# Optimization experiments

Hardware: AMD Instinct MI355X
Metric: run time of the kernel (lower is better)

The kernel has to match this reference:

```python
import jax, jax.numpy as jnp
import numpy as np
import math

DIM = 1536
N_HEADS = 12
HEAD_DIM = DIM // N_HEADS  # 128
C = HEAD_DIM // 2          # 64 complex rotation channels
CT = C - 2 * (C // 3)      # 22 temporal channels
CH = C // 3                # 21 height channels
CW = C // 3                # 21 width channels
F, H, W = 3, 30, 52        # video latent grid -> S = 4680
S = F * H * W
B = 1
EPS = 1e-6
NEG = -1e30


def _rope_angles(max_pos, sizes):
    # Wan-style rope_params per axis: theta_j = 10000^(-j/m) for m complex dims
    parts = []
    pos = jnp.arange(max_pos, dtype=jnp.float32)
    for m in sizes:
        inv = 10000.0 ** (-jnp.arange(m, dtype=jnp.float32) / m)
        parts.append(pos[:, None] * inv[None, :])
    return jnp.concatenate(parts, axis=-1)  # [max_pos, C]


def setup_inputs() -> dict:
    key = jax.random.key(0)
    ks = jax.random.split(key, 6)
    sc = 0.02
    inp = {
        'x': jax.random.normal(ks[0], (B, S, DIM), jnp.float32),
        'seq_lens': jnp.array([S], dtype=jnp.int32),
        'grid_sizes': jnp.array([[F, H, W]], dtype=jnp.int32),
        'freqs': _rope_angles(1024, [CT, CH, CW]),  # [1024, 64] rotation angles
        'Wq': jax.random.normal(ks[1], (DIM, DIM), jnp.float32) * sc,
        'bq': jnp.zeros((DIM,), jnp.float32),
        'Wk': jax.random.normal(ks[2], (DIM, DIM), jnp.float32) * sc,
        'bk': jnp.zeros((DIM,), jnp.float32),
        'Wv': jax.random.normal(ks[3], (DIM, DIM), jnp.float32) * sc,
        'bv': jnp.zeros((DIM,), jnp.float32),
        'Wo': jax.random.normal(ks[4], (DIM, DIM), jnp.float32) * sc,
        'bo': jnp.zeros((DIM,), jnp.float32),
        'gq': jnp.ones((DIM,), jnp.float32),
        'gk': jnp.ones((DIM,), jnp.float32),
    }
    return inp


def _rmsnorm(x, g):
    return x * jax.lax.rsqrt(jnp.mean(x * x, axis=-1, keepdims=True) + EPS) * g


def _apply_rope(x, grid_sizes, freqs):
    # x: [B, S, n, d]; rotate consecutive pairs by 3D (t,h,w) factorized angles.
    b, s, n, d = x.shape
    f = grid_sizes[0, 0]
    h = grid_sizes[0, 1]
    w = grid_sizes[0, 2]
    pos = jnp.arange(s)
    t_idx = pos // (h * w)
    y_idx = (pos % (h * w)) // w
    x_idx = pos % w
    ang = jnp.concatenate([
        freqs[t_idx, :CT],
        freqs[y_idx, CT:CT + CH],
        freqs[x_idx, CT + CH:],
    ], axis=-1)  # [S, C]
    cos = jnp.cos(ang)[None, :, None, :]  # [1, S, 1, C]
    sin = jnp.sin(ang)[None, :, None, :]
    xp = x.reshape(b, s, n, d // 2, 2)
    xr, xi = xp[..., 0], xp[..., 1]
    out_r = xr * cos - xi * sin
    out_i = xr * sin + xi * cos
    return jnp.stack([out_r, out_i], axis=-1).reshape(b, s, n, d)


def reference(x, seq_lens, grid_sizes, freqs, Wq, bq, Wk, bk, Wv, bv, Wo, bo, gq, gk):
    b, s, _ = x.shape
    n, d = N_HEADS, HEAD_DIM
    q = _rmsnorm(x @ Wq.T + bq, gq).reshape(b, s, n, d)
    k = _rmsnorm(x @ Wk.T + bk, gk).reshape(b, s, n, d)
    v = (x @ Wv.T + bv).reshape(b, s, n, d)

    rq = _apply_rope(q, grid_sizes, freqs)
    rk = _apply_rope(k, grid_sizes, freqs)

    # frame-level block-causal mask (block_mask in the original flex_attention)
    frame_seqlen = grid_sizes[0, 1] * grid_sizes[0, 2]
    frame_id = jnp.arange(s) // frame_seqlen
    allowed = frame_id[:, None] >= frame_id[None, :]  # [S, S]

    scale = 1.0 / math.sqrt(d)
    scores = jnp.einsum('bqnd,bknd->bnqk', rq, rk) * scale
    scores = jnp.where(allowed[None, None], scores, NEG)
    attn = jax.nn.softmax(scores, axis=-1)
    out = jnp.einsum('bnqk,bknd->bqnd', attn, v).reshape(b, s, n * d)
    return out @ Wo.T + bo
```

## Files before the change

kernel.cpp:

```cpp
#include <hip/hip_runtime.h>
#include <hip/hip_bf16.h>
#include <math.h>
#include <stdint.h>

#define S_LEN 4680
#define DIMSZ 1536
#define NH    12
#define HD    128
#define FRAME 1560
#define NGRP  74
#define PANH  (NGRP * 8192)
#define NSLOT 150

typedef _Float16 f16;
typedef _Float16 f16x8 __attribute__((ext_vector_type(8)));
typedef _Float16 f16x4 __attribute__((ext_vector_type(4)));
typedef _Float16 f16x2 __attribute__((ext_vector_type(2)));
typedef __fp16   fp16x2 __attribute__((ext_vector_type(2)));
typedef float    f32x4  __attribute__((ext_vector_type(4)));
typedef float    f32x16 __attribute__((ext_vector_type(16)));
typedef int      v2i    __attribute__((ext_vector_type(2)));

__device__ __forceinline__ void async16(const void* g, void* l) {
    __builtin_amdgcn_global_load_lds((const __attribute__((address_space(1))) void*)g,
                                     (__attribute__((address_space(3))) void*)l, 16, 0, 0);
}

__device__ __forceinline__ float fexp2(float x) {
#if __has_builtin(__builtin_amdgcn_exp2f)
    return __builtin_amdgcn_exp2f(x);
#else
    return exp2f(x);
#endif
}

union PkCast { fp16x2 v; int i; };
union FragCast { int w[4]; f16x8 v; };

__global__ __launch_bounds__(256) void cast_all(const float* __restrict__ x,
                                                const float* __restrict__ wq,
                                                const float* __restrict__ wk,
                                                const float* __restrict__ wv,
                                                const float* __restrict__ wo,
                                                f16* __restrict__ xh,
                                                f16* __restrict__ wh) {
    int y = blockIdx.y;
    int i = blockIdx.x * 256 + threadIdx.x;
    if (y == 0) {
        if (i < (S_LEN * DIMSZ) / 4) {
            float4 v = ((const float4*)x)[i];
            f16x4 h; h[0]=(f16)v.x; h[1]=(f16)v.y; h[2]=(f16)v.z; h[3]=(f16)v.w;
            ((f16x4*)xh)[i] = h;
        }
    } else {
        const int nW4 = (DIMSZ * DIMSZ) / 4;
        if (i < nW4) {
            const float* src = (y==1)?wq:(y==2)?wk:(y==3)?wv:wo;
            float4 v = ((const float4*)src)[i];
            f16x4 h; h[0]=(f16)v.x; h[1]=(f16)v.y; h[2]=(f16)v.z; h[3]=(f16)v.w;
            ((f16x4*)wh)[(size_t)(y-1)*nW4 + i] = h;
        }
    }
}

__global__ __launch_bounds__(256) void gemm_qkv(const f16* __restrict__ A,
                                                const f16* __restrict__ Bq,
                                                const f16* __restrict__ Bk,
                                                const f16* __restrict__ Bv,
                                                const float* __restrict__ bq,
                                                const float* __restrict__ bk,
                                                const float* __restrict__ bv,
                                                f16* __restrict__ preq,
                                                f16* __restrict__ prek,
                                                f16* __restrict__ vtp) {
    int z = blockIdx.z;
    const f16* B = (z==0) ? Bq : (z==1) ? Bk : Bv;
    const float* bias = (z==0) ? bq : (z==1) ? bk : bv;

    __shared__ __align__(16) f16 Al[128 * 64];
    __shared__ __align__(16) f16 Bl[128 * 64];
    int tid = threadIdx.x;
    int lane = tid & 63, wv = tid >> 6;
    int l16 = lane & 15, quad = lane >> 4;
    int wr = (wv >> 1) * 64, wc = (wv & 1) * 64;
    int m0 = blockIdx.x * 128, n0 = blockIdx.y * 128;

    f32x4 acc[4][4] = {};

    for (int kb = 0; kb < DIMSZ; kb += 64) {
        __syncthreads();
#pragma unroll
        for (int j = 0; j < 4; j++) {
            int s = j * 256 + wv * 64 + lane;
            int r = s >> 3, cc = s & 7;
            const f16* src = A + (size_t)min(m0 + r, S_LEN - 1) * DIMSZ + kb + ((cc ^ (r & 7)) << 3);
            async16(src, (char*)Al + (j * 4096 + wv * 1024));
        }
#pragma unroll
        for (int j = 0; j < 4; j++) {
            int s = j * 256 + wv * 64 + lane;
            int r = s >> 3, cc = s & 7;
            const f16* src = B + (size_t)(n0 + r) * DIMSZ + kb + ((cc ^ (r & 7)) << 3);
            async16(src, (char*)Bl + (j * 4096 + wv * 1024));
        }
        __builtin_amdgcn_s_waitcnt(0x0f70);
        __syncthreads();

#pragma unroll
        for (int kc = 0; kc < 2; kc++) {
            f16x8 af[4], bf[4];
#pragma unroll
            for (int i = 0; i < 4; i++) {
                int ar = wr + i * 16 + l16;
                af[i] = *(const f16x8*)((const char*)Al + ar * 128 + (((kc * 4 + quad) ^ (ar & 7)) << 4));
                int br = wc + i * 16 + l16;
                bf[i] = *(const f16x8*)((const char*)Bl + br * 128 + (((kc * 4 + quad) ^ (br & 7)) << 4));
            }
#pragma unroll
            for (int mi = 0; mi < 4; mi++)
#pragma unroll
                for (int ni = 0; ni < 4; ni++)
                    acc[mi][ni] = __builtin_amdgcn_mfma_f32_16x16x32_f16(af[mi], bf[ni], acc[mi][ni], 0, 0, 0);
        }
    }

    if (z < 2) {
        f16* C = (z == 0) ? preq : prek;
#pragma unroll
        for (int mi = 0; mi < 4; mi++)
#pragma unroll
            for (int ni = 0; ni < 4; ni++) {
                int col = n0 + wc + ni * 16 + l16;
                float bv_ = bias[col];
#pragma unroll
                for (int r = 0; r < 4; r++) {
                    int row = m0 + wr + mi * 16 + quad * 4 + r;
                    if (row < S_LEN) C[(size_t)row * DIMSZ + col] = (f16)(acc[mi][ni][r] + bv_);
                }
            }
    } else {
#pragma unroll
        for (int mi = 0; mi < 4; mi++)
#pragma unroll
            for (int ni = 0; ni < 4; ni++) {
                int col  = n0 + wc + ni * 16 + l16;
                int vhead = col >> 7, d = col & 127;
                int base = m0 + wr + mi * 16 + quad * 4;
                if (base < S_LEN) {
                    float bv_ = bias[col];
                    f16x4 h;
#pragma unroll
                    for (int r = 0; r < 4; r++) h[r] = (f16)(acc[mi][ni][r] + bv_);
                    size_t off = (size_t)vhead * PANH + (size_t)(base >> 6) * 8192
                               + ((base >> 3) & 7) * 1024 + d * 8 + (base & 7);
                    *(f16x4*)(vtp + off) = h;
                }
            }
    }
}

__global__ __launch_bounds__(256) void norm_rope(const f16* __restrict__ preq,
                                                 const f16* __restrict__ prek,
                                                 const float* __restrict__ gq,
                                                 const float* __restrict__ gk,
                                                 const float* __restrict__ freqs,
                                                 f16* __restrict__ Qp,
                                                 f16* __restrict__ Kp) {
    int s = blockIdx.x, which = blockIdx.y;
    int t = threadIdx.x;
    const f16* pre = which ? prek : preq;
    const float* g = which ? gk : gq;
    f16* dst = which ? Kp : Qp;
    const f16* row = pre + (size_t)s * DIMSZ + t * 6;

    float v[6];
    float ss = 0.f;
#pragma unroll
    for (int i = 0; i < 3; i++) {
        f16x2 hp = *(const f16x2*)(row + 2 * i);
        v[2*i] = (float)hp[0]; v[2*i+1] = (float)hp[1];
        ss += v[2*i]*v[2*i] + v[2*i+1]*v[2*i+1];
    }
#pragma unroll
    for (int off = 32; off; off >>= 1) ss += __shfl_xor(ss, off);
    __shared__ float red[4];
    if ((t & 63) == 0) red[t >> 6] = ss;
    __syncthreads();
    float tot = red[0] + red[1] + red[2] + red[3];
    float rms = rsqrtf(tot * (1.0f / DIMSZ) + 1e-6f);

    int tpos = s / FRAME;
    int rem  = s % FRAME;
    int ypos = rem / 52;
    int xpos = s % 52;

#pragma unroll
    for (int u = 0; u < 3; u++) {
        int c = t * 6 + u * 2;
        int head = c >> 7;
        int d = c & 127;
        int j = d >> 1;
        int idx = (j < 22) ? tpos : ((j < 43) ? ypos : xpos);
        float ang = freqs[idx * 64 + j];
        float sn, cs;
        __sincosf(ang, &sn, &cs);
        float vr = v[u * 2]     * rms * g[c];
        float vi = v[u * 2 + 1] * rms * g[c + 1];
        f16* o = dst + (size_t)head * PANH + (size_t)(s >> 6) * 8192
               + (d >> 3) * 512 + (s & 63) * 8 + (d & 7);
        o[0] = (f16)(vr * cs - vi * sn);
        o[1] = (f16)(vr * sn + vi * cs);
    }
}

__global__ __launch_bounds__(128, 2) void attn_part(const f16* __restrict__ Qp,
                                                    const f16* __restrict__ Kp,
                                                    const f16* __restrict__ Vp,
                                                    f16* __restrict__ Opart,
                                                    float* __restrict__ lpart) {
    int bx = blockIdx.x, head = blockIdx.y;
    int t, c, NC2;
    if (bx < 24)      { t = bx >> 1;             c = bx & 1;       NC2 = 2; }
    else if (bx < 72) { t = 12 + ((bx - 24) >> 2); c = (bx - 24) & 3; NC2 = 4; }
    else              { t = 24 + (bx - 72) / 6;  c = (bx - 72) % 6; NC2 = 6; }

    int qlast = min(t * 128 + 127, S_LEN - 1);
    int nfrm  = qlast / FRAME + 1;
    int kvend = nfrm * FRAME; if (kvend > S_LEN) kvend = S_LEN;
    int nG    = (kvend + 63) >> 6;
    int g0 = (c * nG) / NC2, g1 = ((c + 1) * nG) / NC2;
    int limB = ((t * 128) / FRAME + 1) * FRAME;

    int tid = threadIdx.x, lane = tid & 63, wv = tid >> 6;
    int l31 = lane & 31, lh = lane >> 5;
    int qw = t * 128 + wv * 64;

    __shared__ __align__(16) char smem[32768];
    const char* smc = smem;

    const f16* Qg = Qp + ((size_t)head * NGRP + (qw >> 6)) * 8192;
    f16x8 bqf[2][8];
#pragma unroll
    for (int nt = 0; nt < 2; nt++)
#pragma unroll
        for (int ks = 0; ks < 8; ks++) {
            f16x8 vq = *(const f16x8*)(Qg + (2 * ks + lh) * 512 + (l31 + 32 * nt) * 8);
            bqf[nt][ks] = vq * (f16)0.12752044581f;
        }

    int lim[2];
#pragma unroll
    for (int nt = 0; nt < 2; nt++) {
        int q = qw + l31 + 32 * nt;
        lim[nt] = (q / FRAME + 1) * FRAME;
    }

    f32x16 oacc[4][2] = {};
    float lp[2] = {0.f, 0.f};

    int koff = lh * 1024 + l31 * 16;
    int voff = lh * 2048 + l31 * 16;

    const f16* Kh = Kp + (size_t)head * NGRP * 8192;
    const f16* Vh = Vp + (size_t)head * NGRP * 8192;

    for (int g = g0; g < g1; g++) {
        int kb = g * 64;
#pragma unroll
        for (int i = 0; i < 8; i++) {
            int s = i * 2 + wv;
            async16(Kh + (size_t)g * 8192 + s * 512 + lane * 8,
                    (char*)smem + s * 1024 + lane * 16);
        }
#pragma unroll
        for (int i = 0; i < 8; i++) {
            int s = i * 2 + wv;
            async16(Vh + (size_t)g * 8192 + s * 512 + lane * 8,
                    (char*)smem + 16384 + s * 1024 + lane * 16);
        }
        __builtin_amdgcn_s_waitcnt(0x0f70);
        __builtin_amdgcn_s_barrier();

        bool domask = (kb + 64 > limB);

#pragma unroll
        for (int kt = 0; kt < 2; kt++) {
            f32x16 sc0 = {}, sc1 = {};
            __builtin_amdgcn_s_setprio(1);
#pragma unroll
            for (int h = 0; h < 2; h++) {
                f16x8 ka[4];
#pragma unroll
                for (int i = 0; i < 4; i++)
                    ka[i] = *(const f16x8*)(smc + koff + (h * 4 + i) * 2048 + kt * 512);
#pragma unroll
                for (int i = 0; i < 4; i++) {
                    sc0 = __builtin_amdgcn_mfma_f32_32x32x16_f16(ka[i], bqf[0][h*4+i], sc0, 0, 0, 0);
                    sc1 = __builtin_amdgcn_mfma_f32_32x32x16_f16(ka[i], bqf[1][h*4+i], sc1, 0, 0, 0);
                }
            }
            __builtin_amdgcn_s_setprio(0);

            int w[2][8];
            int keyb = kb + kt * 32 + 4 * lh;
#pragma unroll
            for (int nt = 0; nt < 2; nt++) {
#pragma unroll
                for (int p = 0; p < 8; p++) {
                    const int r0 = 2 * p;
                    float s0 = (nt == 0) ? sc0[r0]     : sc1[r0];
                    float s1 = (nt == 0) ? sc0[r0 + 1] : sc1[r0 + 1];
                    if (domask) {
                        int k0 = keyb + (r0 & 3) + 8 * (r0 >> 2);
                        if (k0     >= lim[nt]) s0 = -1e30f;
                        if (k0 + 1 >= lim[nt]) s1 = -1e30f;
                    }
                    float p0 = fexp2(s0), p1 = fexp2(s1);
                    lp[nt] += p0 + p1;
                    PkCast pk; pk.v = __builtin_amdgcn_cvt_pkrtz(p0, p1);
                    w[nt][p] = pk.i;
                }
            }

            f16x8 pb[2][2];
#pragma unroll
            for (int nt = 0; nt < 2; nt++)
#pragma unroll
                for (int ks = 0; ks < 2; ks++) {
                    FragCast fc;
#if __has_builtin(__builtin_amdgcn_permlane32_swap)
                    v2i r02 = __builtin_amdgcn_permlane32_swap(w[nt][4*ks+0], w[nt][4*ks+2], false, false);
                    v2i r13 = __builtin_amdgcn_permlane32_swap(w[nt][4*ks+1], w[nt][4*ks+3], false, false);
                    fc.w[0] = r02.x; fc.w[1] = r13.x; fc.w[2] = r02.y; fc.w[3] = r13.y;
#else
                    int w0 = w[nt][4*ks], w1 = w[nt][4*ks+1], w2 = w[nt][4*ks+2], w3 = w[nt][4*ks+3];
                    fc.w[0] = lh ? __shfl_xor(w2, 32) : w0;
                    fc.w[1] = lh ? __shfl_xor(w3, 32) : w1;
                    fc.w[2] = lh ? w2 : __shfl_xor(w0, 32);
                    fc.w[3] = lh ? w3 : __shfl_xor(w1, 32);
#endif
                    pb[nt][ks] = fc.v;
                }

            __builtin_amdgcn_s_setprio(1);
#pragma unroll
            for (int mt = 0; mt < 4; mt++)
#pragma unroll
                for (int ks = 0; ks < 2; ks++) {
                    f16x8 va = *(const f16x8*)(smc + 16384 + voff + kt * 8192 + ks * 4096 + mt * 512);
                    oacc[mt][0] = __builtin_amdgcn_mfma_f32_32x32x16_f16(va, pb[0][ks], oacc[mt][0], 0, 0, 0);
                    oacc[mt][1] = __builtin_amdgcn_mfma_f32_32x32x16_f16(va, pb[1][ks], oacc[mt][1], 0, 0, 0);
                }
            __builtin_amdgcn_s_setprio(0);
        }

        __builtin_amdgcn_s_barrier();
    }

    float lt[2], linv[2];
#pragma unroll
    for (int nt = 0; nt < 2; nt++) {
        float l = lp[nt] + __shfl_xor(lp[nt], 32);
        lt[nt] = l;
        linv[nt] = (l > 0.f) ? 1.f / l : 0.f;
    }

    __syncthreads();
    char* ob = (char*)smem + wv * 16384;
#pragma unroll
    for (int mt = 0; mt < 4; mt++)
#pragma unroll
        for (int nt = 0; nt < 2; nt++) {
            int qloc = l31 + 32 * nt;
#pragma unroll
            for (int g4 = 0; g4 < 4; g4++) {
                f16x4 hv;
#pragma unroll
                for (int r = 0; r < 4; r++) hv[r] = (f16)(oacc[mt][nt][g4 * 4 + r] * linv[nt]);
                int c16 = g4 + 4 * mt;
                *(f16x4*)(ob + qloc * 256 + ((c16 ^ (qloc & 7)) << 4) + lh * 8) = hv;
            }
        }
    __syncthreads();

    size_t obase = ((size_t)(head * NSLOT + bx) * 128 + wv * 64) * HD;
#pragma unroll
    for (int a = 0; a < 4; a++)
#pragma unroll
        for (int b = 0; b < 4; b++) {
            int qloc = a * 16 + (lane >> 2);
            int c16  = (lane & 3) + 4 * b;
            f16x8 vv = *(const f16x8*)(ob + qloc * 256 + ((c16 ^ (qloc & 7)) << 4));
            *(f16x8*)(Opart + obase + (size_t)qloc * HD + c16 * 8) = vv;
        }

    if (lane < 32) {
        size_t lbase = (size_t)(head * NSLOT + bx) * 128 + wv * 64;
        lpart[lbase + l31]      = lt[0];
        lpart[lbase + l31 + 32] = lt[1];
    }
}

__global__ __launch_bounds__(256) void combine(const f16* __restrict__ Opart,
                                               const float* __restrict__ lpart,
                                               f16* __restrict__ AO) {
    int gid = blockIdx.x * 256 + threadIdx.x;
    if (gid >= S_LEN * NH * 16) return;
    int dc = gid & 15;
    int head = (gid >> 4) % NH;
    int q = gid / (NH * 16);
    int tt = q >> 7, qloc = q & 127;
    int base, nchunk;
    if (tt < 12)      { base = 2 * tt;             nchunk = 2; }
    else if (tt < 24) { base = 24 + 4 * (tt - 12); nchunk = 4; }
    else              { base = 72 + 6 * (tt - 24); nchunk = 6; }

    float sum[8] = {};
    float ls = 0.f;
    for (int c = 0; c < nchunk; c++) {
        size_t sbase = (size_t)(head * NSLOT + base + c) * 128 + qloc;
        float l = lpart[sbase];
        if (l > 0.f) {
            f16x8 o = *(const f16x8*)(Opart + sbase * HD + dc * 8);
#pragma unroll
            for (int j = 0; j < 8; j++) sum[j] += (float)o[j] * l;
            ls += l;
        }
    }
    float invl = 1.f / ls;
    f16x8 r;
#pragma unroll
    for (int j = 0; j < 8; j++) r[j] = (f16)(sum[j] * invl);
    *(f16x8*)(AO + (size_t)q * DIMSZ + head * HD + dc * 8) = r;
}

__global__ __launch_bounds__(256) void gemm_lds(const f16* __restrict__ A,
                                                const f16* __restrict__ B,
                                                const float* __restrict__ bias,
                                                float* __restrict__ C) {
    __shared__ __align__(16) f16 Al[128 * 64];
    __shared__ __align__(16) f16 Bl[128 * 64];
    int tid = threadIdx.x;
    int lane = tid & 63, wv = tid >> 6;
    int l16 = lane & 15, quad = lane >> 4;
    int wr = (wv >> 1) * 64, wc = (wv & 1) * 64;
    int m0 = blockIdx.x * 128, n0 = blockIdx.y * 128;

    f32x4 acc[4][4] = {};

    for (int kb = 0; kb < DIMSZ; kb += 64) {
        __syncthreads();
#pragma unroll
        for (int j = 0; j < 4; j++) {
            int s = j * 256 + wv * 64 + lane;
            int r = s >> 3, cc = s & 7;
            const f16* src = A + (size_t)min(m0 + r, S_LEN - 1) * DIMSZ + kb + ((cc ^ (r & 7)) << 3);
            async16(src, (char*)Al + (j * 4096 + wv * 1024));
        }
#pragma unroll
        for (int j = 0; j < 4; j++) {
            int s = j * 256 + wv * 64 + lane;
            int r = s >> 3, cc = s & 7;
            const f16* src = B + (size_t)(n0 + r) * DIMSZ + kb + ((cc ^ (r & 7)) << 3);
            async16(src, (char*)Bl + (j * 4096 + wv * 1024));
        }
        __builtin_amdgcn_s_waitcnt(0x0f70);
        __syncthreads();

#pragma unroll
        for (int kc = 0; kc < 2; kc++) {
            f16x8 af[4], bf[4];
#pragma unroll
            for (int i = 0; i < 4; i++) {
                int ar = wr + i * 16 + l16;
                af[i] = *(const f16x8*)((const char*)Al + ar * 128 + (((kc * 4 + quad) ^ (ar & 7)) << 4));
                int br = wc + i * 16 + l16;
                bf[i] = *(const f16x8*)((const char*)Bl + br * 128 + (((kc * 4 + quad) ^ (br & 7)) << 4));
            }
#pragma unroll
            for (int mi = 0; mi < 4; mi++)
#pragma unroll
                for (int ni = 0; ni < 4; ni++)
                    acc[mi][ni] = __builtin_amdgcn_mfma_f32_16x16x32_f16(af[mi], bf[ni], acc[mi][ni], 0, 0, 0);
        }
    }

#pragma unroll
    for (int mi = 0; mi < 4; mi++)
#pragma unroll
        for (int ni = 0; ni < 4; ni++) {
            int col = n0 + wc + ni * 16 + l16;
            float bv = bias[col];
#pragma unroll
            for (int r = 0; r < 4; r++) {
                int row = m0 + wr + mi * 16 + quad * 4 + r;
                if (row < S_LEN) C[(size_t)row * DIMSZ + col] = acc[mi][ni][r] + bv;
            }
        }
}

extern "C" void kernel_launch(void* const* d_in, const int* in_sizes, int n_in,
                              void* d_out, int out_size, void* d_ws, size_t ws_size,
                              hipStream_t stream) {
    const float* x     = (const float*)d_in[0];
    const float* freqs = (const float*)d_in[3];
    const float* Wq = (const float*)d_in[4];
    const float* bq = (const float*)d_in[5];
    const float* Wk = (const float*)d_in[6];
    const float* bk = (const float*)d_in[7];
    const float* Wv = (const float*)d_in[8];
    const float* bv = (const float*)d_in[9];
    const float* Wo = (const float*)d_in[10];
    const float* bo = (const float*)d_in[11];
    const float* gq = (const float*)d_in[12];
    const float* gk = (const float*)d_in[13];
    float* out = (float*)d_out;

    char* ws = (char*)d_ws;
    const size_t SZ_XH  = (size_t)S_LEN * DIMSZ * 2;
    const size_t SZ_W   = (size_t)DIMSZ * DIMSZ * 2;
    const size_t SZ_PAN = (size_t)NH * PANH * 2;
    const size_t SZ_OP  = (size_t)NH * NSLOT * 128 * HD * 2;

    size_t off = 0;
    f16* xh   = (f16*)(ws + off); off += SZ_XH;
    f16* wqh  = (f16*)(ws + off); off += 4 * SZ_W;
    f16* wkh  = wqh + (size_t)DIMSZ * DIMSZ;
    f16* wvh  = wkh + (size_t)DIMSZ * DIMSZ;
    f16* woh  = wvh + (size_t)DIMSZ * DIMSZ;
    f16* Qpan = (f16*)(ws + off); off += SZ_PAN;
    f16* Kpan = (f16*)(ws + off); off += SZ_PAN;
    f16* Vpan = (f16*)(ws + off); off += SZ_PAN;
    f16* AO   = Qpan;
    f16*   preq  = (f16*)(ws + off);
    f16*   prek  = preq + (size_t)S_LEN * DIMSZ;
    f16*   Opart = (f16*)(ws + off);
    float* lpart = (float*)(ws + off + SZ_OP);

    cast_all<<<dim3(7020, 5), 256, 0, stream>>>(x, Wq, Wk, Wv, Wo, xh, wqh);

    gemm_qkv<<<dim3(37, 12, 3), 256, 0, stream>>>(xh, wqh, wkh, wvh, bq, bk, bv,
                                                  preq, prek, Vpan);

    norm_rope<<<dim3(S_LEN, 2), 256, 0, stream>>>(preq, prek, gq, gk, freqs, Qpan, Kpan);

    attn_part<<<dim3(NSLOT, 12), 128, 0, stream>>>(Qpan, Kpan, Vpan, Opart, lpart);
    combine<<<(S_LEN * NH * 16 + 255) / 256, 256, 0, stream>>>(Opart, lpart, AO);

    gemm_lds<<<dim3(37, 12), 256, 0, stream>>>(AO, woh, bo, out);
}
```

Before: 493.9 us.

## Double-buffer K/V tiles in LDS at 32-key granularity with async prefetch

```diff
diff --git a/kernel.cpp b/kernel.cpp
--- a/kernel.cpp
+++ b/kernel.cpp
@@ -236,7 +236,6 @@
     int qw = t * 128 + wv * 64;
 
     __shared__ __align__(16) char smem[32768];
-    const char* smc = smem;
 
     const f16* Qg = Qp + ((size_t)head * NGRP + (qw >> 6)) * 8192;
     f16x8 bqf[2][8];
@@ -258,104 +257,123 @@
     f32x16 oacc[4][2] = {};
     float lp[2] = {0.f, 0.f};
 
-    int koff = lh * 1024 + l31 * 16;
+    int koff = lh * 512 + l31 * 16;
     int voff = lh * 2048 + l31 * 16;
 
     const f16* Kh = Kp + (size_t)head * NGRP * 8192;
     const f16* Vh = Vp + (size_t)head * NGRP * 8192;
 
-    for (int g = g0; g < g1; g++) {
-        int kb = g * 64;
-#pragma unroll
-        for (int i = 0; i < 8; i++) {
-            int s = i * 2 + wv;
-            async16(Kh + (size_t)g * 8192 + s * 512 + lane * 8,
-                    (char*)smem + s * 1024 + lane * 16);
-        }
-#pragma unroll
-        for (int i = 0; i < 8; i++) {
-            int s = i * 2 + wv;
-            async16(Vh + (size_t)g * 8192 + s * 512 + lane * 8,
-                    (char*)smem + 16384 + s * 1024 + lane * 16);
-        }
-        __builtin_amdgcn_s_waitcnt(0x0f70);
+    int sg0 = 2 * g0, sg1 = 2 * g1;
+
+#define STAGE_SG(sg_, b_)                                                        \
+    {                                                                            \
+        int _sg = (sg_);                                                         \
+        size_t _kb = (size_t)(_sg >> 1) * 8192 + (_sg & 1) * 256;                \
+        const f16* _vg = Vh + (size_t)(_sg >> 1) * 8192 + (_sg & 1) * 4096;      \
+        _Pragma("unroll")                                                        \
+        for (int j = 0; j < 4; j++) {                                            \
+            int sl = j * 2 + wv;                                                 \
+            async16(Kh + _kb + (size_t)(sl * 2 + lh) * 512 + l31 * 8,            \
+                    (char*)smem + (b_) * 8192 + sl * 1024 + lane * 16);          \
+        }                                                                        \
+        _Pragma("unroll")                                                        \
+        for (int j = 0; j < 4; j++) {                                            \
+            int sl = j * 2 + wv;                                                 \
+            async16(_vg + sl * 512 + lane * 8,                                   \
+                    (char*)smem + 16384 + (b_) * 8192 + sl * 1024 + lane * 16);  \
+        }                                                                        \
+    }
+
+    STAGE_SG(sg0, 0);
+
+    int cur = 0;
+    for (int sg = sg0; sg < sg1; sg++) {
+        int kb = sg * 32;
+
+        if (sg + 1 < sg1) {
+            STAGE_SG(sg + 1, cur ^ 1);
+            asm volatile("s_waitcnt vmcnt(8)" ::: "memory");
+        } else {
+            asm volatile("s_waitcnt vmcnt(0)" ::: "memory");
+        }
         __builtin_amdgcn_s_barrier();
 
-        bool domask = (kb + 64 > limB);
-
-#pragma unroll
-        for (int kt = 0; kt < 2; kt++) {
-            f32x16 sc0 = {}, sc1 = {};
-            __builtin_amdgcn_s_setprio(1);
-#pragma unroll
-            for (int h = 0; h < 2; h++) {
-                f16x8 ka[4];
-#pragma unroll
-                for (int i = 0; i < 4; i++)
-                    ka[i] = *(const f16x8*)(smc + koff + (h * 4 + i) * 2048 + kt * 512);
-#pragma unroll
-                for (int i = 0; i < 4; i++) {
-                    sc0 = __builtin_amdgcn_mfma_f32_32x32x16_f16(ka[i], bqf[0][h*4+i], sc0, 0, 0, 0);
-                    sc1 = __builtin_amdgcn_mfma_f32_32x32x16_f16(ka[i], bqf[1][h*4+i], sc1, 0, 0, 0);
+        const char* smcK = (const char*)smem + cur * 8192;
+        const char* smcV = (const char*)smem + 16384 + cur * 8192;
+        bool domask = (kb + 32 > limB);
+
+        f32x16 sc0 = {}, sc1 = {};
+        __builtin_amdgcn_s_setprio(1);
+#pragma unroll
+        for (int h = 0; h < 2; h++) {
+            f16x8 ka[4];
+#pragma unroll
+            for (int i = 0; i < 4; i++)
+                ka[i] = *(const f16x8*)(smcK + koff + (h * 4 + i) * 1024);
+#pragma unroll
+            for (int i = 0; i < 4; i++) {
+                sc0 = __builtin_amdgcn_mfma_f32_32x32x16_f16(ka[i], bqf[0][h*4+i], sc0, 0, 0, 0);
+                sc1 = __builtin_amdgcn_mfma_f32_32x32x16_f16(ka[i], bqf[1][h*4+i], sc1, 0, 0, 0);
+            }
+        }
+        __builtin_amdgcn_s_setprio(0);
+
+        int w[2][8];
+        int keyb = kb + 4 * lh;
+#pragma unroll
+        for (int nt = 0; nt < 2; nt++) {
+#pragma unroll
+            for (int p = 0; p < 8; p++) {
+                const int r0 = 2 * p;
+                float s0 = (nt == 0) ? sc0[r0]     : sc1[r0];
+                float s1 = (nt == 0) ? sc0[r0 + 1] : sc1[r0 + 1];
+                if (domask) {
+                    int k0 = keyb + (r0 & 3) + 8 * (r0 >> 2);
+                    if (k0     >= lim[nt]) s0 = -1e30f;
+                    if (k0 + 1 >= lim[nt]) s1 = -1e30f;
                 }
-            }
-            __builtin_amdgcn_s_setprio(0);
-
-            int w[2][8];
-            int keyb = kb + kt * 32 + 4 * lh;
-#pragma unroll
-            for (int nt = 0; nt < 2; nt++) {
-#pragma unroll
-                for (int p = 0; p < 8; p++) {
-                    const int r0 = 2 * p;
-                    float s0 = (nt == 0) ? sc0[r0]     : sc1[r0];
-                    float s1 = (nt == 0) ? sc0[r0 + 1] : sc1[r0 + 1];
-                    if (domask) {
-                        int k0 = keyb + (r0 & 3) + 8 * (r0 >> 2);
-                        if (k0     >= lim[nt]) s0 = -1e30f;
-                        if (k0 + 1 >= lim[nt]) s1 = -1e30f;
-                    }
-                    float p0 = fexp2(s0), p1 = fexp2(s1);
-                    lp[nt] += p0 + p1;
-                    PkCast pk; pk.v = __builtin_amdgcn_cvt_pkrtz(p0, p1);
-                    w[nt][p] = pk.i;
-                }
-            }
-
-            f16x8 pb[2][2];
-#pragma unroll
-            for (int nt = 0; nt < 2; nt++)
-#pragma unroll
-                for (int ks = 0; ks < 2; ks++) {
-                    FragCast fc;
+                float p0 = fexp2(s0), p1 = fexp2(s1);
+                lp[nt] += p0 + p1;
+                PkCast pk; pk.v = __builtin_amdgcn_cvt_pkrtz(p0, p1);
+                w[nt][p] = pk.i;
+            }
+        }
+
+        f16x8 pb[2][2];
+#pragma unroll
+        for (int nt = 0; nt < 2; nt++)
+#pragma unroll
+            for (int ks = 0; ks < 2; ks++) {
+                FragCast fc;
 #if __has_builtin(__builtin_amdgcn_permlane32_swap)
-                    v2i r02 = __builtin_amdgcn_permlane32_swap(w[nt][4*ks+0], w[nt][4*ks+2], false, false);
-                    v2i r13 = __builtin_amdgcn_permlane32_swap(w[nt][4*ks+1], w[nt][4*ks+3], false, false);
-                    fc.w[0] = r02.x; fc.w[1] = r13.x; fc.w[2] = r02.y; fc.w[3] = r13.y;
+                v2i r02 = __builtin_amdgcn_permlane32_swap(w[nt][4*ks+0], w[nt][4*ks+2], false, false);
+                v2i r13 = __builtin_amdgcn_permlane32_swap(w[nt][4*ks+1], w[nt][4*ks+3], false, false);
+                fc.w[0] = r02.x; fc.w[1] = r13.x; fc.w[2] = r02.y; fc.w[3] = r13.y;
 #else
-                    int w0 = w[nt][4*ks], w1 = w[nt][4*ks+1], w2 = w[nt][4*ks+2], w3 = w[nt][4*ks+3];
-                    fc.w[0] = lh ? __shfl_xor(w2, 32) : w0;
-                    fc.w[1] = lh ? __shfl_xor(w3, 32) : w1;
-                    fc.w[2] = lh ? w2 : __shfl_xor(w0, 32);
-                    fc.w[3] = lh ? w3 : __shfl_xor(w1, 32);
+                int w0 = w[nt][4*ks], w1 = w[nt][4*ks+1], w2 = w[nt][4*ks+2], w3 = w[nt][4*ks+3];
+                fc.w[0] = lh ? __shfl_xor(w2, 32) : w0;
+                fc.w[1] = lh ? __shfl_xor(w3, 32) : w1;
+                fc.w[2] = lh ? w2 : __shfl_xor(w0, 32);
+                fc.w[3] = lh ? w3 : __shfl_xor(w1, 32);
 #endif
-                    pb[nt][ks] = fc.v;
-                }
-
-            __builtin_amdgcn_s_setprio(1);
-#pragma unroll
-            for (int mt = 0; mt < 4; mt++)
-#pragma unroll
-                for (int ks = 0; ks < 2; ks++) {
-                    f16x8 va = *(const f16x8*)(smc + 16384 + voff + kt * 8192 + ks * 4096 + mt * 512);
-                    oacc[mt][0] = __builtin_amdgcn_mfma_f32_32x32x16_f16(va, pb[0][ks], oacc[mt][0], 0, 0, 0);
-                    oacc[mt][1] = __builtin_amdgcn_mfma_f32_32x32x16_f16(va, pb[1][ks], oacc[mt][1], 0, 0, 0);
-                }
-            __builtin_amdgcn_s_setprio(0);
-        }
+                pb[nt][ks] = fc.v;
+            }
+
+        __builtin_amdgcn_s_setprio(1);
+#pragma unroll
+        for (int mt = 0; mt < 4; mt++)
+#pragma unroll
+            for (int ks = 0; ks < 2; ks++) {
+                f16x8 va = *(const f16x8*)(smcV + ks * 4096 + voff + mt * 512);
+                oacc[mt][0] = __builtin_amdgcn_mfma_f32_32x32x16_f16(va, pb[0][ks], oacc[mt][0], 0, 0, 0);
+                oacc[mt][1] = __builtin_amdgcn_mfma_f32_32x32x16_f16(va, pb[1][ks], oacc[mt][1], 0, 0, 0);
+            }
+        __builtin_amdgcn_s_setprio(0);
 
         __builtin_amdgcn_s_barrier();
-    }
+        cur ^= 1;
+    }
+#undef STAGE_SG
 
     float lt[2], linv[2];
 #pragma unroll
```

Result: no change. 488.7 us (-1.1%).
